# Performance work log

Hardware: AMD Instinct MI355X
Metric: run time of the kernel (lower is better)

## Reference

```python
import jax, jax.numpy as jnp
import numpy as np

B, C, S, N, V = 8, 16, 512, 512, 128
EPS = 1e-5

def setup_inputs() -> dict:
    key = jax.random.key(0)
    ks = jax.random.split(key, 9)
    def u(k, shape, scale):
        return jax.random.uniform(k, shape, jnp.float32, -scale, scale)
    attn_scale = 12 * np.sqrt(3.0 / (S * N * V))      # custom attn_init for query / key.left / value2
    xav_vs = np.sqrt(6.0 / (V + S))                    # xavier_uniform for (C, V, S) or (C, S, V)
    xav_nv = np.sqrt(6.0 / (N + V))                    # xavier_uniform for (C, N, V)
    return {
        "x": jax.random.normal(ks[0], (B, C, S, N), jnp.float32),
        "wq": u(ks[1], (C, N, V), attn_scale),          # query weight (other_features=S)
        "k_left": u(ks[2], (C, V, S), attn_scale),      # key left (attn_init)
        "k_right": u(ks[3], (C, N, V), xav_nv),         # key right (xavier)
        "v1_left": u(ks[4], (C, V, S), xav_vs),         # value1 left (xavier, attn_init=False)
        "v1_right": u(ks[5], (C, N, V), attn_scale),    # value1 right (attn_init scale)
        "v2_w": u(ks[6], (C, V, S), attn_scale),        # value2 weight (other_features=N)
        "gamma": jnp.ones((C,), jnp.float32),
        "beta": jnp.zeros((C,), jnp.float32),
    }

def batch_scaler(y, gamma, beta):
    # normalize over dims (0, 2, 3); per-channel affine
    mean = jnp.mean(y, axis=(0, 2, 3), keepdims=True)
    var = jnp.mean(jnp.square(y - mean), axis=(0, 2, 3), keepdims=True)
    yhat = (y - mean) * jax.lax.rsqrt(var + EPS)
    return yhat * gamma[None, :, None, None] + beta[None, :, None, None]

def reference(x, wq, k_left, k_right, v1_left, v1_right, v2_w, gamma, beta):
    # x: [B,C,S,N]
    q = jnp.matmul(x, wq)                               # [B,C,S,V]
    k = jnp.matmul(jnp.matmul(k_left, x), k_right)       # (C,V,S)@x -> [B,C,V,N] @ (C,N,V) -> [B,C,V,V]
    attn = jax.nn.softmax(jnp.einsum('bcsv,bcwv->bcsw', q, k), axis=-1)  # q @ k^T, softmax last dim
    v1 = jnp.matmul(jnp.matmul(v1_left, x), v1_right)    # [B,C,V,V]
    v2 = jnp.matmul(v2_w, x)                             # [B,C,V,N]
    v = jnp.matmul(v1, v2)                               # [B,C,V,N]
    y = x + jnp.matmul(attn, v)                          # [B,C,S,N]
    return batch_scaler(y, gamma, beta)
```

## Files before the change

kernel.cpp:

```cpp
#include <hip/hip_runtime.h>
#include <math.h>


typedef short  bf16x8 __attribute__((ext_vector_type(8)));
typedef short  short8 __attribute__((ext_vector_type(8)));
typedef float  f32x4  __attribute__((ext_vector_type(4)));

__device__ __forceinline__ unsigned short f2bf(float f) {
    union { float f; unsigned u; } v; v.f = f;
    return (unsigned short)((v.u + 0x7FFF + ((v.u >> 16) & 1)) >> 16);
}
__device__ __forceinline__ float bf2f(unsigned short u) {
    union { unsigned u; float f; } v; v.u = (unsigned)u << 16; return v.f;
}

__device__ __forceinline__ void gload16(const void* g, void* l)
{
    __builtin_amdgcn_global_load_lds(
        (const __attribute__((address_space(1))) void*)g,
        (__attribute__((address_space(3))) void*)l, 16, 0, 0);
}

constexpr size_t OB_XB   = 0;
constexpr size_t OB_XT   = OB_XB  + 67108864;
constexpr size_t OB_KLB  = OB_XT  + 67108864;
constexpr size_t OB_V1LB = OB_KLB + 2097152;
constexpr size_t OB_V2WB = OB_V1LB+ 2097152;
constexpr size_t OB_WQT  = OB_V2WB+ 2097152;
constexpr size_t OB_KRT  = OB_WQT + 2097152;
constexpr size_t OB_V1RT = OB_KRT + 2097152;
constexpr size_t OB_BUF  = OB_V1RT+ 2097152;
constexpr size_t OB_V2T  = OB_BUF + 33554432;
constexpr size_t OB_KM   = OB_V2T + 16777216;
constexpr size_t OB_V1M  = OB_KM  + 4194304;
constexpr size_t OB_ATT  = OB_V1M + 4194304;
constexpr size_t OB_VT   = OB_ATT + 16777216;
constexpr size_t OB_ST   = OB_VT  + 16777216;

template<int NSTEPS, int MF, int NF>
__device__ __forceinline__ void mmcore(const char* __restrict__ Ab, int ldaB,
                                       const char* __restrict__ Bb, int ldbB,
                                       f32x4 (&acc)[MF][NF],
                                       char* __restrict__ smA, char* __restrict__ smB,
                                       int wm, int wn)
{
    const int tid = threadIdx.x;
    const int w = tid >> 6, l = tid & 63, g = l >> 4, lr = l & 15;
    const int rl = l >> 3, ch = l & 7;

#pragma unroll 1
    for (int t = 0; t < NSTEPS; ++t) {
#pragma unroll
        for (int j = 0; j < 4; ++j) {
            const int row = w * 32 + j * 8 + rl;
            gload16(Ab + (size_t)row * ldaB + t * 128 + ((ch ^ (row & 7)) * 16),
                    smA + (w * 32 + j * 8) * 128);
        }
#pragma unroll
        for (int j = 0; j < 4; ++j) {
            const int row = w * 32 + j * 8 + rl;
            gload16(Bb + (size_t)row * ldbB + t * 128 + ((ch ^ (row & 7)) * 16),
                    smB + (w * 32 + j * 8) * 128);
        }
        __syncthreads();
#pragma unroll
        for (int ks = 0; ks < 2; ++ks) {
            bf16x8 av[MF], bv[NF];
            const int cc = ks * 4 + g;
#pragma unroll
            for (int i = 0; i < MF; ++i) { int rw = wm + i * 16 + lr;
                av[i] = *(const bf16x8*)(smA + rw * 128 + ((cc ^ (rw & 7)) * 16)); }
#pragma unroll
            for (int j = 0; j < NF; ++j) { int rw = wn + j * 16 + lr;
                bv[j] = *(const bf16x8*)(smB + rw * 128 + ((cc ^ (rw & 7)) * 16)); }
#pragma unroll
            for (int i = 0; i < MF; ++i)
#pragma unroll
                for (int j = 0; j < NF; ++j)
                    acc[i][j] = __builtin_amdgcn_mfma_f32_16x16x32_bf16(av[i], bv[j], acc[i][j], 0, 0, 0);
        }
        __syncthreads();
    }
}

__device__ __forceinline__ void epi_write_rm(const f32x4 (&acc)[4][4], char* sm)
{
    const int tid = threadIdx.x, w = tid >> 6, l = tid & 63, g = l >> 4, lr = l & 15;
    const int wm = (w >> 1) * 64, wn = (w & 1) * 64;
#pragma unroll
    for (int i = 0; i < 4; ++i)
#pragma unroll
        for (int j = 0; j < 4; ++j) {
            const int row = wm + i * 16 + g * 4, col = wn + j * 16 + lr;
#pragma unroll
            for (int r = 0; r < 4; ++r)
                *(unsigned short*)(sm + (row + r) * 272 + col * 2) = f2bf(acc[i][j][r]);
        }
}

__device__ __forceinline__ void epi_write_tr(const f32x4 (&acc)[4][4], char* sm)
{
    const int tid = threadIdx.x, w = tid >> 6, l = tid & 63, g = l >> 4, lr = l & 15;
    const int wm = (w >> 1) * 64, wn = (w & 1) * 64;
#pragma unroll
    for (int i = 0; i < 4; ++i)
#pragma unroll
        for (int j = 0; j < 4; ++j) {
            const int rv = wm + i * 16 + g * 4, cn = wn + j * 16 + lr;
            ushort4 pk = make_ushort4(f2bf(acc[i][j][0]), f2bf(acc[i][j][1]),
                                      f2bf(acc[i][j][2]), f2bf(acc[i][j][3]));
            *(ushort4*)(sm + cn * 272 + rv * 2) = pk;
        }
}

__device__ __forceinline__ void epi_flush(const char* sm, unsigned short* gout, int ldg)
{
    const int tid = threadIdx.x;
    const int r0 = tid >> 4, q = tid & 15;
#pragma unroll
    for (int rep = 0; rep < 8; ++rep) {
        const int row = rep * 16 + r0;
        *(short8*)((short*)gout + (size_t)row * ldg + q * 8) =
            *(const short8*)(sm + row * 272 + q * 16);
    }
    __syncthreads();
}

__global__ __launch_bounds__(256) void k_prep(const float* __restrict__ kl,
                                              const float* __restrict__ v1l,
                                              const float* __restrict__ v2w,
                                              const float* __restrict__ wq,
                                              const float* __restrict__ kr,
                                              const float* __restrict__ v1r,
                                              unsigned short* __restrict__ klb,
                                              unsigned short* __restrict__ v1lb,
                                              unsigned short* __restrict__ v2wb,
                                              unsigned short* __restrict__ wqt,
                                              unsigned short* __restrict__ krt,
                                              unsigned short* __restrict__ v1rt,
                                              float* __restrict__ stats)
{
    __shared__ float tl[64][65];
    const int id = blockIdx.x, tid = threadIdx.x;
    if (id == 0 && tid < 64) stats[tid] = 0.f;
    if (id < 192) {
        const int sel = id >> 6, blk = id & 63;
        const float* src = sel == 0 ? kl : sel == 1 ? v1l : v2w;
        unsigned short* dst = sel == 0 ? klb : sel == 1 ? v1lb : v2wb;
#pragma unroll
        for (int r = 0; r < 4; ++r) {
            const int i = blk * 1024 + r * 256 + tid;
            float4 v = ((const float4*)src)[i];
            ((ushort4*)dst)[i] = make_ushort4(f2bf(v.x), f2bf(v.y), f2bf(v.z), f2bf(v.w));
        }
        return;
    }
    const int id2 = id - 192;
    const int p = id2 >> 4, rem = id2 & 15, by = rem >> 1, bx = rem & 1;
    const int widx = p >> 4, c = p & 15;
    const float* s = (widx == 0 ? wq : widx == 1 ? kr : v1r) + (size_t)c * 65536;
    unsigned short* d = (widx == 0 ? wqt : widx == 1 ? krt : v1rt) + (size_t)c * 65536;
    const int r0 = by * 64, c0 = bx * 64;
    const int rr = tid >> 4, cc = (tid & 15) * 4;
#pragma unroll
    for (int rep = 0; rep < 4; ++rep) {
        int row = rep * 16 + rr;
        float4 v = *(const float4*)(s + (size_t)(r0 + row) * 128 + c0 + cc);
        tl[cc + 0][row] = v.x; tl[cc + 1][row] = v.y; tl[cc + 2][row] = v.z; tl[cc + 3][row] = v.w;
    }
    __syncthreads();
#pragma unroll
    for (int rep = 0; rep < 4; ++rep) {
        int crow = rep * 16 + rr;
        *(ushort4*)(d + (size_t)(c0 + crow) * 512 + r0 + cc) =
            make_ushort4(f2bf(tl[crow][cc]), f2bf(tl[crow][cc + 1]),
                         f2bf(tl[crow][cc + 2]), f2bf(tl[crow][cc + 3]));
    }
}

__global__ __launch_bounds__(256) void ktransx(const float* __restrict__ x,
                                               unsigned short* __restrict__ xt)
{
    __shared__ float tl[64][65];
    const int bc = blockIdx.z;
    const int r0 = blockIdx.y * 64, c0 = blockIdx.x * 64;
    const float* src = x + (size_t)bc * 262144;
    const int tid = threadIdx.x;
    const int rr = tid >> 3, q8 = (tid & 7) * 8;
#pragma unroll
    for (int rep = 0; rep < 2; ++rep) {
        const int row = rep * 32 + rr;
        float4 a = *(const float4*)(src + (size_t)(r0 + row) * 512 + c0 + q8);
        float4 b = *(const float4*)(src + (size_t)(r0 + row) * 512 + c0 + q8 + 4);
        tl[q8 + 0][row] = a.x; tl[q8 + 1][row] = a.y; tl[q8 + 2][row] = a.z; tl[q8 + 3][row] = a.w;
        tl[q8 + 4][row] = b.x; tl[q8 + 5][row] = b.y; tl[q8 + 6][row] = b.z; tl[q8 + 7][row] = b.w;
    }
    __syncthreads();
#pragma unroll
    for (int rep = 0; rep < 2; ++rep) {
        const int crow = rep * 32 + rr;
        short8 o;
#pragma unroll
        for (int k = 0; k < 8; ++k) o[k] = (short)f2bf(tl[crow][q8 + k]);
        *(short8*)(xt + (size_t)bc * 262144 + (size_t)(c0 + crow) * 512 + r0 + q8) = o;
    }
}

__global__ __launch_bounds__(256, 2) void k_wx(const unsigned short* __restrict__ klb,
                                               const unsigned short* __restrict__ v1lb,
                                               const unsigned short* __restrict__ v2wb,
                                               const unsigned short* __restrict__ xt,
                                               unsigned short* __restrict__ bufb,
                                               unsigned short* __restrict__ v2t)
{
    __shared__ char smem[34816];
    char* smA = smem; char* smB = smem + 16384;
    const int mt = blockIdx.x >> 2, n0 = blockIdx.x & 3, bc = blockIdx.y, c = bc & 15;
    const unsigned short* W = mt == 0 ? klb : mt == 1 ? v1lb : v2wb;
    const char* Bb = (const char*)(xt + (size_t)bc * 262144 + (size_t)n0 * 65536);
    const int w = threadIdx.x >> 6;
    f32x4 acc[4][4] = {};
    mmcore<8, 4, 4>((const char*)(W + (size_t)c * 65536), 1024, Bb, 1024, acc, smA, smB,
                    (w >> 1) * 64, (w & 1) * 64);
    if (mt < 2) {
        epi_write_rm(acc, smem);
        __syncthreads();
        epi_flush(smem, bufb + (size_t)bc * 131072 + (size_t)mt * 65536 + n0 * 128, 512);
    } else {
        epi_write_tr(acc, smem);
        __syncthreads();
        epi_flush(smem, v2t + (size_t)bc * 65536 + (size_t)n0 * 16384, 128);
    }
}

__global__ __launch_bounds__(256, 2) void k_kr(const unsigned short* __restrict__ bufb,
                                               const unsigned short* __restrict__ krt,
                                               const unsigned short* __restrict__ v1rt,
                                               unsigned short* __restrict__ kmat,
                                               unsigned short* __restrict__ v1m)
{
    __shared__ char smem[34816];
    char* smA = smem; char* smB = smem + 16384;
    const int mt = blockIdx.x, bc = blockIdx.y, c = bc & 15;
    const int w = threadIdx.x >> 6;
    f32x4 acc[4][4] = {};
    mmcore<8, 4, 4>((const char*)(bufb + (size_t)bc * 131072 + (size_t)mt * 65536), 1024,
                    (const char*)((mt ? v1rt : krt) + (size_t)c * 65536), 1024, acc, smA, smB,
                    (w >> 1) * 64, (w & 1) * 64);
    epi_write_rm(acc, smem);
    __syncthreads();
    epi_flush(smem, (mt ? v1m : kmat) + (size_t)bc * 16384, 128);
}

__global__ __launch_bounds__(256, 2) void k_qat(const float* __restrict__ x,
                                                const unsigned short* __restrict__ wqt,
                                                const unsigned short* __restrict__ kmat,
                                                unsigned short* __restrict__ attn)
{
    __shared__ char smem[49152];
    char* smA  = smem;
    char* smB  = smem + 16384;
    char* qlds = smem;
    char* smB2 = smem + 32768;
    const int mt = blockIdx.x, bc = blockIdx.y, c = bc & 15;
    const int tid = threadIdx.x, w = tid >> 6, l = tid & 63, g = l >> 4, lr = l & 15;
    const int rl = l >> 3, ch = l & 7;
    const int wm = (w >> 1) * 64, wn = (w & 1) * 64;

    f32x4 acc[4][4] = {};
    {
        const float* Ax = x + (size_t)bc * 262144 + (size_t)(mt * 128) * 512;
        const char* Bw = (const char*)(wqt + (size_t)c * 65536);
        const int ar = tid >> 4, fq = tid & 15;
#pragma unroll 1
        for (int t = 0; t < 8; ++t) {
#pragma unroll
            for (int j = 0; j < 4; ++j) {
                const int row = w * 32 + j * 8 + rl;
                gload16(Bw + (size_t)row * 1024 + t * 128 + ((ch ^ (row & 7)) * 16),
                        smB + (w * 32 + j * 8) * 128);
            }
            float4 fr[8];
#pragma unroll
            for (int it = 0; it < 8; ++it) {
                const int row = it * 16 + ar;
                fr[it] = *(const float4*)(Ax + (size_t)row * 512 + t * 64 + fq * 4);
            }
#pragma unroll
            for (int it = 0; it < 8; ++it) {
                const int row = it * 16 + ar;
                ushort4 o = make_ushort4(f2bf(fr[it].x), f2bf(fr[it].y),
                                         f2bf(fr[it].z), f2bf(fr[it].w));
                *(ushort4*)(smA + row * 128 + (((fq >> 1) ^ (row & 7)) * 16) + (fq & 1) * 8) = o;
            }
            __syncthreads();
#pragma unroll
            for (int ks = 0; ks < 2; ++ks) {
                const int cc2 = ks * 4 + g;
                bf16x8 av[4], bv[4];
#pragma unroll
                for (int i = 0; i < 4; ++i) { const int rw = wm + i * 16 + lr;
                    av[i] = *(const bf16x8*)(smA + rw * 128 + ((cc2 ^ (rw & 7)) * 16)); }
#pragma unroll
                for (int j = 0; j < 4; ++j) { const int rw = wn + j * 16 + lr;
                    bv[j] = *(const bf16x8*)(smB + rw * 128 + ((cc2 ^ (rw & 7)) * 16)); }
#pragma unroll
                for (int i = 0; i < 4; ++i)
#pragma unroll
                    for (int j = 0; j < 4; ++j)
                        acc[i][j] = __builtin_amdgcn_mfma_f32_16x16x32_bf16(av[i], bv[j], acc[i][j], 0, 0, 0);
            }
            __syncthreads();
        }
    }
    {
        const int t = wn >> 6;
#pragma unroll
        for (int i = 0; i < 4; ++i)
#pragma unroll
            for (int j = 0; j < 4; ++j) {
                const int k6 = j * 16 + lr;
                const int chunk = k6 >> 3, eb = (k6 & 7) << 1;
#pragma unroll
                for (int r = 0; r < 4; ++r) {
                    const int row = wm + i * 16 + g * 4 + r;
                    *(unsigned short*)(qlds + t * 16384 + row * 128 +
                                       ((chunk ^ (row & 7)) << 4) + eb) = f2bf(acc[i][j][r]);
                }
            }
    }
    __syncthreads();

    f32x4 acc2[2][8] = {};
    const char* Kb = (const char*)(kmat + (size_t)bc * 16384);
#pragma unroll
    for (int t = 0; t < 2; ++t) {
#pragma unroll
        for (int j = 0; j < 4; ++j) {
            const int row = w * 32 + j * 8 + rl;
            gload16(Kb + (size_t)row * 256 + t * 128 + ((ch ^ (row & 7)) * 16),
                    smB2 + (w * 32 + j * 8) * 128);
        }
        __syncthreads();
#pragma unroll
        for (int ks = 0; ks < 2; ++ks) {
            const int cc2 = ks * 4 + g;
            bf16x8 av[2], bv[8];
#pragma unroll
            for (int i = 0; i < 2; ++i) { const int rw = w * 32 + i * 16 + lr;
                av[i] = *(const bf16x8*)(qlds + t * 16384 + rw * 128 + ((cc2 ^ (rw & 7)) * 16)); }
#pragma unroll
            for (int j = 0; j < 8; ++j) { const int rw = j * 16 + lr;
                bv[j] = *(const bf16x8*)(smB2 + rw * 128 + ((cc2 ^ (rw & 7)) * 16)); }
#pragma unroll
            for (int i = 0; i < 2; ++i)
#pragma unroll
                for (int j = 0; j < 8; ++j)
                    acc2[i][j] = __builtin_amdgcn_mfma_f32_16x16x32_bf16(av[i], bv[j], acc2[i][j], 0, 0, 0);
        }
        __syncthreads();
    }

    char* wsl = smem + w * 8704;
    unsigned short* ob = attn + (size_t)bc * 65536 + (size_t)(mt * 128 + w * 32) * 128;
#pragma unroll
    for (int i = 0; i < 2; ++i)
#pragma unroll
        for (int r = 0; r < 4; ++r) {
            float mx = -3e38f;
#pragma unroll
            for (int fj = 0; fj < 8; ++fj) mx = fmaxf(mx, acc2[i][fj][r]);
#pragma unroll
            for (int d = 1; d < 16; d <<= 1) mx = fmaxf(mx, __shfl_xor(mx, d));
            float s = 0.f, e[8];
#pragma unroll
            for (int fj = 0; fj < 8; ++fj) { e[fj] = __expf(acc2[i][fj][r] - mx); s += e[fj]; }
#pragma unroll
            for (int d = 1; d < 16; d <<= 1) s += __shfl_xor(s, d);
            const float inv = 1.f / s;
            const int rowh = i * 16 + g * 4 + r;
#pragma unroll
            for (int fj = 0; fj < 8; ++fj)
                *(unsigned short*)(wsl + rowh * 272 + (fj * 16 + lr) * 2) = f2bf(e[fj] * inv);
        }
#pragma unroll
    for (int rep = 0; rep < 8; ++rep) {
        const int row = rep * 4 + (l >> 4);
        *(short8*)((short*)ob + (size_t)row * 128 + (l & 15) * 8) =
            *(const short8*)(wsl + row * 272 + (l & 15) * 16);
    }
}

__global__ __launch_bounds__(256, 2) void k_v(const unsigned short* __restrict__ v2t,
                                              const unsigned short* __restrict__ v1m,
                                              unsigned short* __restrict__ vt)
{
    __shared__ char smem[34816];
    char* smA = smem; char* smB = smem + 16384;
    const int mt = blockIdx.x, bc = blockIdx.y;
    const int w = threadIdx.x >> 6;
    f32x4 acc[4][4] = {};
    mmcore<2, 4, 4>((const char*)(v2t + (size_t)bc * 65536 + (size_t)mt * 16384), 256,
                    (const char*)(v1m + (size_t)bc * 16384), 256, acc, smA, smB,
                    (w >> 1) * 64, (w & 1) * 64);
    epi_write_rm(acc, smem);
    __syncthreads();
    epi_flush(smem, vt + (size_t)bc * 65536 + (size_t)mt * 16384, 128);
}

__global__ __launch_bounds__(256, 2) void k_y(const unsigned short* __restrict__ attn,
                                              const unsigned short* __restrict__ vt,
                                              const float* __restrict__ x,
                                              unsigned short* __restrict__ yb,
                                              float* __restrict__ stats)
{
    __shared__ char smem[34816];
    __shared__ float r1[4], r2[4];
    char* smA = smem; char* smB = smem + 16384;
    const int nx = blockIdx.x, my = blockIdx.y, bc = blockIdx.z, c = bc & 15;
    const int tid = threadIdx.x, w = tid >> 6, l = tid & 63, g = l >> 4, lr = l & 15;
    f32x4 acc[4][4] = {};
    mmcore<2, 4, 4>((const char*)(attn + (size_t)bc * 65536 + (size_t)my * 16384), 256,
                    (const char*)(vt + (size_t)bc * 65536 + (size_t)nx * 16384), 256, acc, smA, smB,
                    (w >> 1) * 64, (w & 1) * 64);
    const float* xw = x + (size_t)bc * 262144 + (size_t)my * 128 * 512 + nx * 128;
    const int wm = (w >> 1) * 64, wn = (w & 1) * 64;
    float lsum = 0.f, lss = 0.f;
#pragma unroll
    for (int i = 0; i < 4; ++i)
#pragma unroll
        for (int j = 0; j < 4; ++j)
#pragma unroll
            for (int r = 0; r < 4; ++r) {
                const int row = wm + i * 16 + g * 4 + r, col = wn + j * 16 + lr;
                const float yv = acc[i][j][r] + xw[(size_t)row * 512 + col];
                lsum += yv; lss += yv * yv;
                *(unsigned short*)(smem + row * 272 + col * 2) = f2bf(yv);
            }
#pragma unroll
    for (int d = 32; d >= 1; d >>= 1) { lsum += __shfl_xor(lsum, d); lss += __shfl_xor(lss, d); }
    if (l == 0) { r1[w] = lsum; r2[w] = lss; }
    __syncthreads();
    epi_flush(smem, yb + (size_t)bc * 262144 + (size_t)my * 128 * 512 + nx * 128, 512);
    if (tid == 0) {
        atomicAdd(&stats[c * 2 + 0], r1[0] + r1[1] + r1[2] + r1[3]);
        atomicAdd(&stats[c * 2 + 1], r2[0] + r2[1] + r2[2] + r2[3]);
    }
}

__global__ __launch_bounds__(256) void k_norm(const unsigned short* __restrict__ yb,
                                              float* __restrict__ out,
                                              const float* __restrict__ stats,
                                              const float* __restrict__ gamma,
                                              const float* __restrict__ beta)
{
    __shared__ float ssc[16], ssh[16];
    if (threadIdx.x < 16) {
        const int c = threadIdx.x;
        const float cnt  = 2097152.f;
        const float mean = stats[c * 2 + 0] / cnt;
        const float var  = stats[c * 2 + 1] / cnt - mean * mean;
        const float sc   = rsqrtf(var + 1e-5f) * gamma[c];
        ssc[c] = sc;
        ssh[c] = beta[c] - mean * sc;
    }
    __syncthreads();
    const int tot = 4194304;
    for (int i = blockIdx.x * 256 + threadIdx.x; i < tot; i += gridDim.x * 256) {
        const long e = (long)i * 8;
        const int c = (int)(e >> 18) & 15;
        const float sc = ssc[c];
        const float sh = ssh[c];
        short8 v = ((const short8*)yb)[i];
        float4 o0, o1;
        o0.x = bf2f((unsigned short)v[0]) * sc + sh;
        o0.y = bf2f((unsigned short)v[1]) * sc + sh;
        o0.z = bf2f((unsigned short)v[2]) * sc + sh;
        o0.w = bf2f((unsigned short)v[3]) * sc + sh;
        o1.x = bf2f((unsigned short)v[4]) * sc + sh;
        o1.y = bf2f((unsigned short)v[5]) * sc + sh;
        o1.z = bf2f((unsigned short)v[6]) * sc + sh;
        o1.w = bf2f((unsigned short)v[7]) * sc + sh;
        ((float4*)out)[(size_t)i * 2 + 0] = o0;
        ((float4*)out)[(size_t)i * 2 + 1] = o1;
    }
}

extern "C" void kernel_launch(void* const* d_in, const int* in_sizes, int n_in,
                              void* d_out, int out_size, void* d_ws, size_t ws_size,
                              hipStream_t stream)
{
    (void)in_sizes; (void)n_in; (void)out_size; (void)ws_size;
    const float* x     = (const float*)d_in[0];
    const float* wq    = (const float*)d_in[1];
    const float* kl    = (const float*)d_in[2];
    const float* kr    = (const float*)d_in[3];
    const float* v1l   = (const float*)d_in[4];
    const float* v1r   = (const float*)d_in[5];
    const float* v2w   = (const float*)d_in[6];
    const float* gamma = (const float*)d_in[7];
    const float* beta  = (const float*)d_in[8];
    float* out = (float*)d_out;
    char*  ws  = (char*)d_ws;

    unsigned short* yb   = (unsigned short*)(ws + OB_XB);
    unsigned short* xt   = (unsigned short*)(ws + OB_XT);
    unsigned short* klb  = (unsigned short*)(ws + OB_KLB);
    unsigned short* v1lb = (unsigned short*)(ws + OB_V1LB);
    unsigned short* v2wb = (unsigned short*)(ws + OB_V2WB);
    unsigned short* wqt  = (unsigned short*)(ws + OB_WQT);
    unsigned short* krt  = (unsigned short*)(ws + OB_KRT);
    unsigned short* v1rt = (unsigned short*)(ws + OB_V1RT);
    unsigned short* bufb = (unsigned short*)(ws + OB_BUF);
    unsigned short* v2t  = (unsigned short*)(ws + OB_V2T);
    unsigned short* kmat = (unsigned short*)(ws + OB_KM);
    unsigned short* v1m  = (unsigned short*)(ws + OB_V1M);
    unsigned short* attn = (unsigned short*)(ws + OB_ATT);
    unsigned short* vt   = (unsigned short*)(ws + OB_VT);
    float*          st   = (float*)(ws + OB_ST);

    hipLaunchKernelGGL(k_prep,  dim3(960),       dim3(256), 0, stream,
                       kl, v1l, v2w, wq, kr, v1r, klb, v1lb, v2wb, wqt, krt, v1rt, st);
    hipLaunchKernelGGL(ktransx, dim3(8, 8, 128), dim3(256), 0, stream, x, xt);
    hipLaunchKernelGGL(k_wx,    dim3(12, 128),   dim3(256), 0, stream, klb, v1lb, v2wb, xt, bufb, v2t);
    hipLaunchKernelGGL(k_kr,    dim3(2, 128),    dim3(256), 0, stream, bufb, krt, v1rt, kmat, v1m);
    hipLaunchKernelGGL(k_qat,   dim3(4, 128),    dim3(256), 0, stream, x, wqt, kmat, attn);
    hipLaunchKernelGGL(k_v,     dim3(4, 128),    dim3(256), 0, stream, v2t, v1m, vt);
    hipLaunchKernelGGL(k_y,     dim3(4, 4, 128), dim3(256), 0, stream, attn, vt, x, yb, st);
    hipLaunchKernelGGL(k_norm,  dim3(2048),      dim3(256), 0, stream, yb, out, st, gamma, beta);
}
```

Baseline: 245.4 us.

## Fuse x transpose and bf16 conversion into the W@x GEMM kernel

```diff
diff --git a/kernel.cpp b/kernel.cpp
--- a/kernel.cpp
+++ b/kernel.cpp
@@ -178,50 +178,73 @@
     }
 }
 
-__global__ __launch_bounds__(256) void ktransx(const float* __restrict__ x,
-                                               unsigned short* __restrict__ xt)
-{
-    __shared__ float tl[64][65];
-    const int bc = blockIdx.z;
-    const int r0 = blockIdx.y * 64, c0 = blockIdx.x * 64;
-    const float* src = x + (size_t)bc * 262144;
-    const int tid = threadIdx.x;
-    const int rr = tid >> 3, q8 = (tid & 7) * 8;
-#pragma unroll
-    for (int rep = 0; rep < 2; ++rep) {
-        const int row = rep * 32 + rr;
-        float4 a = *(const float4*)(src + (size_t)(r0 + row) * 512 + c0 + q8);
-        float4 b = *(const float4*)(src + (size_t)(r0 + row) * 512 + c0 + q8 + 4);
-        tl[q8 + 0][row] = a.x; tl[q8 + 1][row] = a.y; tl[q8 + 2][row] = a.z; tl[q8 + 3][row] = a.w;
-        tl[q8 + 4][row] = b.x; tl[q8 + 5][row] = b.y; tl[q8 + 6][row] = b.z; tl[q8 + 7][row] = b.w;
-    }
-    __syncthreads();
-#pragma unroll
-    for (int rep = 0; rep < 2; ++rep) {
-        const int crow = rep * 32 + rr;
-        short8 o;
-#pragma unroll
-        for (int k = 0; k < 8; ++k) o[k] = (short)f2bf(tl[crow][q8 + k]);
-        *(short8*)(xt + (size_t)bc * 262144 + (size_t)(c0 + crow) * 512 + r0 + q8) = o;
-    }
-}
-
 __global__ __launch_bounds__(256, 2) void k_wx(const unsigned short* __restrict__ klb,
                                                const unsigned short* __restrict__ v1lb,
                                                const unsigned short* __restrict__ v2wb,
-                                               const unsigned short* __restrict__ xt,
+                                               const float* __restrict__ x,
                                                unsigned short* __restrict__ bufb,
                                                unsigned short* __restrict__ v2t)
 {
     __shared__ char smem[34816];
-    char* smA = smem; char* smB = smem + 16384;
+    char* smA = smem;
+    char* smX = smem + 16384;
     const int mt = blockIdx.x >> 2, n0 = blockIdx.x & 3, bc = blockIdx.y, c = bc & 15;
     const unsigned short* W = mt == 0 ? klb : mt == 1 ? v1lb : v2wb;
-    const char* Bb = (const char*)(xt + (size_t)bc * 262144 + (size_t)n0 * 65536);
-    const int w = threadIdx.x >> 6;
+    const char* Wb = (const char*)(W + (size_t)c * 65536);
+    const float* xs = x + (size_t)bc * 262144 + n0 * 128;
+    const int tid = threadIdx.x, w = tid >> 6, l = tid & 63, g = l >> 4, lr = l & 15;
+    const int rl = l >> 3, ch = l & 7;
+    const int wm = (w >> 1) * 64, wn = (w & 1) * 64;
+    const int nq = (tid & 31) * 4, sp2 = (tid >> 5) * 2;
+
     f32x4 acc[4][4] = {};
-    mmcore<8, 4, 4>((const char*)(W + (size_t)c * 65536), 1024, Bb, 1024, acc, smA, smB,
-                    (w >> 1) * 64, (w & 1) * 64);
+#pragma unroll 1
+    for (int t = 0; t < 8; ++t) {
+#pragma unroll
+        for (int j = 0; j < 4; ++j) {
+            const int row = w * 32 + j * 8 + rl;
+            gload16(Wb + (size_t)row * 1024 + t * 128 + ((ch ^ (row & 7)) * 16),
+                    smA + (w * 32 + j * 8) * 128);
+        }
+#pragma unroll
+        for (int k = 0; k < 4; ++k) {
+            const int sl = k * 16 + sp2;
+            float4 f0 = *(const float4*)(xs + (size_t)(t * 64 + sl) * 512 + nq);
+            float4 f1 = *(const float4*)(xs + (size_t)(t * 64 + sl + 1) * 512 + nq);
+            const unsigned lo0 = f2bf(f0.x), lo1 = f2bf(f0.y), lo2 = f2bf(f0.z), lo3 = f2bf(f0.w);
+            const unsigned hi0 = f2bf(f1.x), hi1 = f2bf(f1.y), hi2 = f2bf(f1.z), hi3 = f2bf(f1.w);
+            char* base = smX + sl * 2;
+            *(unsigned*)(base + (nq + 0) * 136) = lo0 | (hi0 << 16);
+            *(unsigned*)(base + (nq + 1) * 136) = lo1 | (hi1 << 16);
+            *(unsigned*)(base + (nq + 2) * 136) = lo2 | (hi2 << 16);
+            *(unsigned*)(base + (nq + 3) * 136) = lo3 | (hi3 << 16);
+        }
+        __syncthreads();
+#pragma unroll
+        for (int ks = 0; ks < 2; ++ks) {
+            const int cc = ks * 4 + g;
+            bf16x8 av[4], bv[4];
+#pragma unroll
+            for (int i = 0; i < 4; ++i) { const int rw = wm + i * 16 + lr;
+                av[i] = *(const bf16x8*)(smA + rw * 128 + ((cc ^ (rw & 7)) * 16)); }
+#pragma unroll
+            for (int j = 0; j < 4; ++j) {
+                const int n = wn + j * 16 + lr;
+                const char* p = smX + n * 136 + cc * 16;
+                union { unsigned long long u[2]; bf16x8 v; } tmp;
+                tmp.u[0] = *(const unsigned long long*)(p);
+                tmp.u[1] = *(const unsigned long long*)(p + 8);
+                bv[j] = tmp.v;
+            }
+#pragma unroll
+            for (int i = 0; i < 4; ++i)
+#pragma unroll
+                for (int j = 0; j < 4; ++j)
+                    acc[i][j] = __builtin_amdgcn_mfma_f32_16x16x32_bf16(av[i], bv[j], acc[i][j], 0, 0, 0);
+        }
+        __syncthreads();
+    }
+
     if (mt < 2) {
         epi_write_rm(acc, smem);
         __syncthreads();
@@ -504,7 +527,6 @@
     char*  ws  = (char*)d_ws;
 
     unsigned short* yb   = (unsigned short*)(ws + OB_XB);
-    unsigned short* xt   = (unsigned short*)(ws + OB_XT);
     unsigned short* klb  = (unsigned short*)(ws + OB_KLB);
     unsigned short* v1lb = (unsigned short*)(ws + OB_V1LB);
     unsigned short* v2wb = (unsigned short*)(ws + OB_V2WB);
@@ -521,8 +543,7 @@
 
     hipLaunchKernelGGL(k_prep,  dim3(960),       dim3(256), 0, stream,
                        kl, v1l, v2w, wq, kr, v1r, klb, v1lb, v2wb, wqt, krt, v1rt, st);
-    hipLaunchKernelGGL(ktransx, dim3(8, 8, 128), dim3(256), 0, stream, x, xt);
-    hipLaunchKernelGGL(k_wx,    dim3(12, 128),   dim3(256), 0, stream, klb, v1lb, v2wb, xt, bufb, v2t);
+    hipLaunchKernelGGL(k_wx,    dim3(12, 128),   dim3(256), 0, stream, klb, v1lb, v2wb, x, bufb, v2t);
     hipLaunchKernelGGL(k_kr,    dim3(2, 128),    dim3(256), 0, stream, bufb, krt, v1rt, kmat, v1m);
     hipLaunchKernelGGL(k_qat,   dim3(4, 128),    dim3(256), 0, stream, x, wqt, kmat, attn);
     hipLaunchKernelGGL(k_v,     dim3(4, 128),    dim3(256), 0, stream, v2t, v1m, vt);
```

Result: faster. 234.2 us (-4.6%).
